# Kernel optimization log

Hardware: AMD Instinct MI355X
Metric: run time of the kernel (lower is better)

## Reference

```python
import jax, jax.numpy as jnp
import numpy as np

EPS = 1e-5

def setup_inputs() -> dict:
    key = jax.random.key(0)
    k1, k2, k3, k4, k5 = jax.random.split(key, 5)
    B, D, S = 4096, 2048, 16384
    return {
        "x": jax.random.normal(k1, (B, D), dtype=jnp.float32),
        "W_enc": jax.random.normal(k2, (S, D), dtype=jnp.float32) * 0.02,  # encoder.weight [n_sae, n_input]
        "W_dec": jax.random.normal(k3, (D, S), dtype=jnp.float32) * 0.02,  # decoder.weight [n_input, n_sae]
        "pre_bias": jax.random.normal(k4, (D,), dtype=jnp.float32) * 0.01,
        "sae_bias": jax.random.normal(k5, (S,), dtype=jnp.float32) * 0.01,
        "k": 64,
    }

def reference(x, W_enc, W_dec, pre_bias, sae_bias, k):
    # --- pre_process: layer norm (torch.std is unbiased -> ddof=1) ---
    x_mean = jnp.mean(x, axis=-1, keepdims=True)
    std = jnp.std(x, axis=-1, ddof=1, keepdims=True)
    x_ln = (x - x_mean) / (std + EPS)
    # --- encode: latents_pre = (x_ln - pre_bias) @ W_enc^T + sae_bias ---
    pre_activations = (x_ln - pre_bias) @ W_enc.T + sae_bias  # [B, n_sae]
    # --- TopK activation: keep top-k, ReLU them, zero the rest ---
    vals, idx = jax.lax.top_k(pre_activations, k)              # [B, k]
    vals = jax.nn.relu(vals)
    rows = jnp.arange(pre_activations.shape[0])[:, None]       # [B, 1]
    latents = jnp.zeros_like(pre_activations).at[rows, idx].set(vals)
    # --- decode + un-normalize ---
    recons = latents @ W_dec.T + pre_bias                      # [B, n_input]
    recons = recons * std + x_mean
    return pre_activations, latents, recons
```

## Files before the change

### kernel.cpp

```cpp
#include <hip/hip_runtime.h>
#include <cstdint>
#include <cstddef>

#define EPSV 1e-5f
#define CAP 224
#define PAD 16
#define DELTA 0.03f
#define AMBCAP 64

__device__ __forceinline__ unsigned short f2bf(float f) {
  unsigned u = __float_as_uint(f);
  unsigned r = (u + 0x7FFFu + ((u >> 16) & 1u)) >> 16;
  return (unsigned short)r;
}
__device__ __forceinline__ float bf2f(unsigned short h) {
  return __uint_as_float(((unsigned)h) << 16);
}

__global__ __launch_bounds__(256) void ln_kernel(const float* __restrict__ x,
    const float* __restrict__ pre_bias, float* __restrict__ a,
    unsigned short* __restrict__ A2,
    float* __restrict__ stats, int D) {
  const int b = blockIdx.x;
  const int tid = threadIdx.x;
  const float4* x4 = reinterpret_cast<const float4*>(x + (size_t)b * D);
  const float4* pb4 = reinterpret_cast<const float4*>(pre_bias);
  float4* a4 = reinterpret_cast<float4*>(a + (size_t)b * D);
  float4 v0 = x4[tid], v1 = x4[tid + 256];
  float s = v0.x + v0.y + v0.z + v0.w + v1.x + v1.y + v1.z + v1.w;
  float ss = v0.x*v0.x + v0.y*v0.y + v0.z*v0.z + v0.w*v0.w
           + v1.x*v1.x + v1.y*v1.y + v1.z*v1.z + v1.w*v1.w;
#pragma unroll
  for (int off = 1; off < 64; off <<= 1) { s += __shfl_xor(s, off); ss += __shfl_xor(ss, off); }
  __shared__ float wsum[4], wssq[4], bmean, bstd;
  int wave = tid >> 6;
  if ((tid & 63) == 0) { wsum[wave] = s; wssq[wave] = ss; }
  __syncthreads();
  if (tid == 0) {
    float S1 = wsum[0] + wsum[1] + wsum[2] + wsum[3];
    float S2 = wssq[0] + wssq[1] + wssq[2] + wssq[3];
    float mean = S1 / (float)D;
    float var = (S2 - (float)D * mean * mean) / (float)(D - 1);
    float sd = sqrtf(fmaxf(var, 0.f));
    bmean = mean; bstd = sd;
    stats[2*b] = mean; stats[2*b+1] = sd;
  }
  __syncthreads();
  float mean = bmean, rstd = 1.f / (bstd + EPSV);
  float4 p0 = pb4[tid], p1 = pb4[tid + 256];
  float4 o0, o1;
  o0.x = (v0.x - mean) * rstd - p0.x; o0.y = (v0.y - mean) * rstd - p0.y;
  o0.z = (v0.z - mean) * rstd - p0.z; o0.w = (v0.w - mean) * rstd - p0.w;
  o1.x = (v1.x - mean) * rstd - p1.x; o1.y = (v1.y - mean) * rstd - p1.y;
  o1.z = (v1.z - mean) * rstd - p1.z; o1.w = (v1.w - mean) * rstd - p1.w;
  a4[tid] = o0; a4[tid + 256] = o1;
  if (A2) {
    unsigned short* row = A2 + (size_t)b * 2048;
    ushort4 h0 = make_ushort4(f2bf(o0.x), f2bf(o0.y), f2bf(o0.z), f2bf(o0.w));
    ushort4 h1 = make_ushort4(f2bf(o1.x), f2bf(o1.y), f2bf(o1.z), f2bf(o1.w));
    *reinterpret_cast<ushort4*>(row + tid * 4) = h0;
    *reinterpret_cast<ushort4*>(row + 1024 + tid * 4) = h1;
  }
}

__global__ __launch_bounds__(256) void cvt_w_kernel(const float* __restrict__ W,
    unsigned short* __restrict__ W2, int D) {
  const int s = blockIdx.x, tid = threadIdx.x;
  const float4* w4 = reinterpret_cast<const float4*>(W + (size_t)s * D);
  unsigned short* row = W2 + (size_t)s * D;
  float4 v0 = w4[tid * 2], v1 = w4[tid * 2 + 1];
  uint4 p;
  p.x = (unsigned)f2bf(v0.x) | ((unsigned)f2bf(v0.y) << 16);
  p.y = (unsigned)f2bf(v0.z) | ((unsigned)f2bf(v0.w) << 16);
  p.z = (unsigned)f2bf(v1.x) | ((unsigned)f2bf(v1.y) << 16);
  p.w = (unsigned)f2bf(v1.z) | ((unsigned)f2bf(v1.w) << 16);
  *reinterpret_cast<uint4*>(row + tid * 8) = p;
}

typedef __attribute__((ext_vector_type(8))) short bf8;
typedef __attribute__((ext_vector_type(4))) float f32x4;

__device__ __forceinline__ void gload16(const void* g, void* l) {
  __builtin_amdgcn_global_load_lds(
      (const __attribute__((address_space(1))) unsigned int*)g,
      (__attribute__((address_space(3))) unsigned int*)l,
      16, 0, 0);
}

__global__ __launch_bounds__(512) void enc_gemm_bf16(
    const unsigned short* __restrict__ A2,
    const unsigned short* __restrict__ W2,
    const float* __restrict__ sae_bias,
    float* __restrict__ C, int M, int N) {
  __shared__ __align__(16) short As0[128 * 64];
  __shared__ __align__(16) short Bs0[128 * 64];
  __shared__ __align__(16) short As1[128 * 64];
  __shared__ __align__(16) short Bs1[128 * 64];
  const int tid = threadIdx.x;
  const int bn = blockIdx.x, bm = blockIdx.y;
  const int w = tid >> 6, l = tid & 63;

  const unsigned short* gA[2];
  const unsigned short* gB[2];
  int ldsSlot[2];
#pragma unroll
  for (int r = 0; r < 2; ++r) {
    int slot = r * 512 + tid;
    int row = slot >> 3, unit = slot & 7;
    int gcol = (unit ^ (row & 7)) * 8;
    gA[r] = A2 + (size_t)(bm * 128 + row) * 2048 + gcol;
    gB[r] = W2 + (size_t)(bn * 128 + row) * 2048 + gcol;
    ldsSlot[r] = slot * 8;
  }

  const int wm = (w >> 2) * 64, wn = (w & 3) * 32;
  const int r15 = l & 15, b7 = l & 7, u = l >> 4;
  const int colks0 = ((u + 0) ^ b7) * 8;
  const int colks1 = ((u + 4) ^ b7) * 8;
  const int baseA = (wm + r15) * 64;
  const int baseB = (wn + r15) * 64;

  f32x4 acc[4][2];
#pragma unroll
  for (int mi = 0; mi < 4; ++mi)
#pragma unroll
    for (int ni = 0; ni < 2; ++ni) acc[mi][ni] = (f32x4){0.f, 0.f, 0.f, 0.f};

#define STAGE(Adst, Bdst, koff)                                   \
  {                                                               \
    _Pragma("unroll")                                             \
    for (int r = 0; r < 2; ++r) {                                 \
      gload16(gA[r] + (koff), &(Adst)[ldsSlot[r]]);               \
      gload16(gB[r] + (koff), &(Bdst)[ldsSlot[r]]);               \
    }                                                             \
  }

#define COMPUTE(Asrc, Bsrc)                                       \
  {                                                               \
    _Pragma("unroll")                                             \
    for (int ks = 0; ks < 2; ++ks) {                              \
      const int ck = ks ? colks1 : colks0;                        \
      bf8 af[4], bfv[2];                                          \
      _Pragma("unroll")                                           \
      for (int mi = 0; mi < 4; ++mi)                              \
        af[mi] = *reinterpret_cast<const bf8*>(&(Asrc)[baseA + mi * 1024 + ck]); \
      _Pragma("unroll")                                           \
      for (int ni = 0; ni < 2; ++ni)                              \
        bfv[ni] = *reinterpret_cast<const bf8*>(&(Bsrc)[baseB + ni * 1024 + ck]); \
      __builtin_amdgcn_s_setprio(1);                              \
      _Pragma("unroll")                                           \
      for (int mi = 0; mi < 4; ++mi)                              \
        _Pragma("unroll")                                         \
        for (int ni = 0; ni < 2; ++ni)                            \
          acc[mi][ni] = __builtin_amdgcn_mfma_f32_16x16x32_bf16(  \
              af[mi], bfv[ni], acc[mi][ni], 0, 0, 0);             \
      __builtin_amdgcn_s_setprio(0);                              \
    }                                                             \
  }

#define SYNC_TILE()                                               \
  {                                                               \
    asm volatile("s_waitcnt vmcnt(0)" ::: "memory");              \
    __builtin_amdgcn_s_barrier();                                 \
    asm volatile("" ::: "memory");                                \
  }

  STAGE(As0, Bs0, 0);
  SYNC_TILE();

  for (int t = 0; t < 32; t += 2) {
    STAGE(As1, Bs1, (t + 1) * 64);
    COMPUTE(As0, Bs0);
    SYNC_TILE();
    if (t + 2 < 32) STAGE(As0, Bs0, (t + 2) * 64);
    COMPUTE(As1, Bs1);
    SYNC_TILE();
  }
#undef STAGE
#undef COMPUTE
#undef SYNC_TILE

  const int cm = (l >> 4) * 4, cn = l & 15;
  float sb[2];
#pragma unroll
  for (int ni = 0; ni < 2; ++ni)
    sb[ni] = sae_bias[bn * 128 + wn + ni * 16 + cn];
#pragma unroll
  for (int mi = 0; mi < 4; ++mi) {
#pragma unroll
    for (int r = 0; r < 4; ++r) {
      int row = bm * 128 + wm + mi * 16 + cm + r;
      float* Crow = C + (size_t)row * N + bn * 128 + wn;
#pragma unroll
      for (int ni = 0; ni < 2; ++ni)
        Crow[ni * 16 + cn] = acc[mi][ni][r] + sb[ni];
    }
  }
}

#define BM 128
#define BN 128
#define BK 32
#define LDP 136

__global__ __launch_bounds__(256) void enc_gemm_f32(
    const float* __restrict__ A, const float* __restrict__ Bw,
    const float* __restrict__ sae_bias, float* __restrict__ C,
    int M, int N, int K) {
  __shared__ __align__(16) float As[BK * LDP];
  __shared__ __align__(16) float Bs[BK * LDP];
  const int tid = threadIdx.x;
  const int bn = blockIdx.x, bm = blockIdx.y;
  const float* Ab = A + (size_t)bm * BM * K;
  const float* Bb = Bw + (size_t)bn * BN * K;
  float acc[8][8];
#pragma unroll
  for (int i = 0; i < 8; ++i)
#pragma unroll
    for (int j = 0; j < 8; ++j) acc[i][j] = 0.f;
  const int tn = tid & 15, tm = tid >> 4;
  const int lk = tid & 31;
  const int lm4 = (tid >> 5) * 4;
  for (int k0 = 0; k0 < K; k0 += BK) {
#pragma unroll
    for (int i = 0; i < 4; ++i) {
      int mb = i * 32 + lm4;
      float a0 = Ab[(size_t)(mb + 0) * K + k0 + lk];
      float a1 = Ab[(size_t)(mb + 1) * K + k0 + lk];
      float a2 = Ab[(size_t)(mb + 2) * K + k0 + lk];
      float a3 = Ab[(size_t)(mb + 3) * K + k0 + lk];
      *reinterpret_cast<float4*>(&As[lk * LDP + mb]) = make_float4(a0, a1, a2, a3);
      float b0 = Bb[(size_t)(mb + 0) * K + k0 + lk];
      float b1 = Bb[(size_t)(mb + 1) * K + k0 + lk];
      float b2 = Bb[(size_t)(mb + 2) * K + k0 + lk];
      float b3 = Bb[(size_t)(mb + 3) * K + k0 + lk];
      *reinterpret_cast<float4*>(&Bs[lk * LDP + mb]) = make_float4(b0, b1, b2, b3);
    }
    __syncthreads();
#pragma unroll 8
    for (int kk = 0; kk < BK; ++kk) {
      float4 a0 = *reinterpret_cast<const float4*>(&As[kk * LDP + tm * 4]);
      float4 a1 = *reinterpret_cast<const float4*>(&As[kk * LDP + tm * 4 + 64]);
      float4 b0 = *reinterpret_cast<const float4*>(&Bs[kk * LDP + tn * 4]);
      float4 b1 = *reinterpret_cast<const float4*>(&Bs[kk * LDP + tn * 4 + 64]);
      float av[8] = {a0.x, a0.y, a0.z, a0.w, a1.x, a1.y, a1.z, a1.w};
      float bv[8] = {b0.x, b0.y, b0.z, b0.w, b1.x, b1.y, b1.z, b1.w};
#pragma unroll
      for (int ii = 0; ii < 8; ++ii)
#pragma unroll
        for (int jj = 0; jj < 8; ++jj)
          acc[ii][jj] = fmaf(av[ii], bv[jj], acc[ii][jj]);
    }
    __syncthreads();
  }
  float4 sb0 = *reinterpret_cast<const float4*>(sae_bias + bn * BN + tn * 4);
  float4 sb1 = *reinterpret_cast<const float4*>(sae_bias + bn * BN + tn * 4 + 64);
#pragma unroll
  for (int ii = 0; ii < 8; ++ii) {
    int row = bm * BM + (ii < 4 ? tm * 4 + ii : 64 + tm * 4 + ii - 4);
    float* Crow = C + (size_t)row * N + bn * BN;
    float4 o0 = make_float4(acc[ii][0] + sb0.x, acc[ii][1] + sb0.y,
                            acc[ii][2] + sb0.z, acc[ii][3] + sb0.w);
    float4 o1 = make_float4(acc[ii][4] + sb1.x, acc[ii][5] + sb1.y,
                            acc[ii][6] + sb1.z, acc[ii][7] + sb1.w);
    *reinterpret_cast<float4*>(Crow + tn * 4) = o0;
    *reinterpret_cast<float4*>(Crow + tn * 4 + 64) = o1;
  }
}

__device__ __forceinline__ unsigned mapf(float f) {
  unsigned u = __float_as_uint(f);
  return (u & 0x80000000u) ? ~u : (u | 0x80000000u);
}

__global__ __launch_bounds__(256) void topk_select(
    const float* __restrict__ preact, float* __restrict__ latents,
    const int* __restrict__ kp, int* __restrict__ cand, float* __restrict__ candv,
    int* __restrict__ candcnt, int S) {
  const int b = blockIdx.x, tid = threadIdx.x;
  const float4* row4 = reinterpret_cast<const float4*>(preact + (size_t)b * S);
  __shared__ int hist[4096];
  __shared__ int tsum[256];
  __shared__ unsigned sh_pref, sh_thr;
  __shared__ int sh_done, sh_cum, sh_cnt;
  int K = kp[0]; if (K > 192) K = 192;
  const int r = K + PAD;
  if (tid == 0) { sh_done = 0; sh_pref = 0; sh_cum = 0; }
  for (int level = 0; level < 3; ++level) {
    __syncthreads();
    if (sh_done) break;
    const int shift = (level == 0) ? 20 : (level == 1) ? 8 : 0;
    const int width = (level == 2) ? 8 : 12;
    const int nb = 1 << width;
    const unsigned mask = (unsigned)nb - 1;
    for (int i = tid; i < nb; i += 256) hist[i] = 0;
    __syncthreads();
    const unsigned pref = sh_pref;
    for (int i = tid; i < S / 4; i += 256) {
      float4 v = row4[i];
      unsigned uu[4] = {mapf(v.x), mapf(v.y), mapf(v.z), mapf(v.w)};
#pragma unroll
      for (int q = 0; q < 4; ++q) {
        bool ok = (level == 0) || ((uu[q] >> (shift + width)) == pref);
        if (ok) atomicAdd(&hist[(uu[q] >> shift) & mask], 1);
      }
    }
    __syncthreads();
    const int per = nb >> 8;
    int myts = 0;
#pragma unroll 4
    for (int j = 0; j < per; ++j) myts += hist[tid * per + j];
    tsum[tid] = myts;
    __syncthreads();
    for (int o = 1; o < 256; o <<= 1) {
      int v_ = (tid + o < 256) ? tsum[tid + o] : 0;
      __syncthreads();
      tsum[tid] += v_;
      __syncthreads();
    }
    const int rr = r - sh_cum;
    const int sufIncl = tsum[tid];
    const int sufExcl = sufIncl - myts;
    if (sufExcl < rr && rr <= sufIncl) {
      int running = sufExcl;
      for (int j = per - 1; j >= 0; --j) {
        int bb = tid * per + j;
        int c = hist[bb];
        if (running + c >= rr) {
          unsigned npref = (sh_pref << width) | (unsigned)bb;
          int candTotal = sh_cum + running + c;
          sh_pref = npref;
          sh_cum += running;
          if (candTotal <= CAP || level == 2) { sh_thr = npref << shift; sh_done = 1; }
          break;
        }
        running += c;
      }
    }
  }
  __syncthreads();
  const unsigned T = sh_thr;
  if (tid == 0) sh_cnt = 0;
  __syncthreads();
  float4* lat4 = reinterpret_cast<float4*>(latents + (size_t)b * S);
  float4 z = make_float4(0.f, 0.f, 0.f, 0.f);
  for (int i = tid; i < S / 4; i += 256) {
    float4 v = row4[i];
    unsigned uu[4] = {mapf(v.x), mapf(v.y), mapf(v.z), mapf(v.w)};
    float vv[4] = {v.x, v.y, v.z, v.w};
#pragma unroll
    for (int q = 0; q < 4; ++q) {
      if (uu[q] >= T) {
        int p = atomicAdd(&sh_cnt, 1);
        if (p < CAP) { cand[(size_t)b * CAP + p] = i * 4 + q; candv[(size_t)b * CAP + p] = vv[q]; }
      }
    }
    lat4[i] = z;
  }
  __syncthreads();
  if (tid == 0) candcnt[b] = (sh_cnt < CAP) ? sh_cnt : CAP;
}

__global__ __launch_bounds__(256) void topk_refine(
    const float* __restrict__ a, const float* __restrict__ W_enc,
    const float* __restrict__ sae_bias, const int* __restrict__ kp,
    const int* __restrict__ cand, const float* __restrict__ candv,
    const int* __restrict__ candcnt,
    float* __restrict__ latents, int* __restrict__ out_idx, float* __restrict__ out_val,
    int D, int S) {
  const int b = blockIdx.x, tid = threadIdx.x;
  __shared__ float sv[256];
  __shared__ int si[256];
  __shared__ double sv64[256];
  __shared__ double av[AMBCAP];
  __shared__ int agid[AMBCAP];
  __shared__ int sh_amb, sh_nin;
  int K = kp[0]; if (K > 192) K = 192;
  const int cnt = candcnt[b];
  const int wave = tid >> 6, lane = tid & 63;
  const float4* ar4 = reinterpret_cast<const float4*>(a + (size_t)b * D);
  const int nit = D / 256;

  if (tid < cnt) { sv[tid] = candv[(size_t)b * CAP + tid]; si[tid] = cand[(size_t)b * CAP + tid]; }
  else { sv[tid] = -3.0e38f; si[tid] = 0x7FFFFFFF; }
  __syncthreads();
  for (int ksz = 2; ksz <= 256; ksz <<= 1) {
    for (int j = ksz >> 1; j > 0; j >>= 1) {
      int ixj = tid ^ j;
      if (ixj > tid) {
        float v1 = sv[tid], v2 = sv[ixj];
        int i1 = si[tid], i2 = si[ixj];
        bool dirDesc = ((tid & ksz) == 0);
        bool firstBetter = (v1 > v2) || (v1 == v2 && i1 < i2);
        if (dirDesc ? (!firstBetter) : firstBetter) {
          sv[tid] = v2; sv[ixj] = v1; si[tid] = i2; si[ixj] = i1;
        }
      }
      __syncthreads();
    }
  }
  const float vK = sv[K - 1];
  if (tid == 0) { sh_amb = 0; sh_nin = 0; }
  __syncthreads();
  bool isC = tid < cnt;
  if (isC && (sv[tid] > vK + DELTA)) atomicAdd(&sh_nin, 1);
  if (isC && fabsf(sv[tid] - vK) <= DELTA) {
    int p = atomicAdd(&sh_amb, 1);
    if (p < AMBCAP) agid[p] = si[tid];
  }
  __syncthreads();
  const int nAmb = sh_amb, nIn = sh_nin;

  if (nAmb <= AMBCAP) {
    for (int c = wave; c < nAmb; c += 4) {
      int sidx = agid[c];
      const float4* wr4 = reinterpret_cast<const float4*>(W_enc + (size_t)sidx * D);
      double acc = 0.0;
      for (int m = 0; m < nit; ++m) {
        float4 a_ = ar4[m * 64 + lane];
        float4 w_ = wr4[m * 64 + lane];
        acc += (double)a_.x * w_.x + (double)a_.y * w_.y
             + (double)a_.z * w_.z + (double)a_.w * w_.w;
      }
#pragma unroll
      for (int off = 1; off < 64; off <<= 1) acc += __shfl_xor(acc, off);
      if (lane == 0) av[c] = acc + (double)sae_bias[sidx];
    }
    __syncthreads();
    if (tid < AMBCAP && tid >= nAmb) { av[tid] = -1.0e300; agid[tid] = 0x7FFFFFFF; }
    __syncthreads();
    for (int ksz = 2; ksz <= AMBCAP; ksz <<= 1) {
      for (int j = ksz >> 1; j > 0; j >>= 1) {
        int ixj = tid ^ j;
        if (tid < AMBCAP && ixj > tid) {
          double v1 = av[tid], v2 = av[ixj];
          int i1 = agid[tid], i2 = agid[ixj];
          bool dirDesc = ((tid & ksz) == 0);
          bool firstBetter = (v1 > v2) || (v1 == v2 && i1 < i2);
          if (dirDesc ? (!firstBetter) : firstBetter) {
            av[tid] = v2; av[ixj] = v1; agid[tid] = i2; agid[ixj] = i1;
          }
        }
        __syncthreads();
      }
    }
    if (tid < K) {
      int gidx; float val;
      if (tid < nIn) { gidx = si[tid]; val = sv[tid]; }
      else { int c = tid - nIn; gidx = agid[c]; val = (float)av[c]; }
      val = fmaxf(val, 0.f);
      latents[(size_t)b * S + gidx] = val;
      out_idx[(size_t)b * 256 + tid] = gidx;
      out_val[(size_t)b * 256 + tid] = val;
    }
  } else {
    for (int c = wave; c < cnt; c += 4) {
      int sidx = si[c];
      const float4* wr4 = reinterpret_cast<const float4*>(W_enc + (size_t)sidx * D);
      double acc = 0.0;
      for (int m = 0; m < nit; ++m) {
        float4 a_ = ar4[m * 64 + lane];
        float4 w_ = wr4[m * 64 + lane];
        acc += (double)a_.x * w_.x + (double)a_.y * w_.y
             + (double)a_.z * w_.z + (double)a_.w * w_.w;
      }
#pragma unroll
      for (int off = 1; off < 64; off <<= 1) acc += __shfl_xor(acc, off);
      if (lane == 0) sv64[c] = acc + (double)sae_bias[sidx];
    }
    __syncthreads();
    if (tid >= cnt) { sv64[tid] = -1.0e300; si[tid] = 0x7FFFFFFF; }
    __syncthreads();
    for (int ksz = 2; ksz <= 256; ksz <<= 1) {
      for (int j = ksz >> 1; j > 0; j >>= 1) {
        int ixj = tid ^ j;
        if (ixj > tid) {
          double v1 = sv64[tid], v2 = sv64[ixj];
          int i1 = si[tid], i2 = si[ixj];
          bool dirDesc = ((tid & ksz) == 0);
          bool firstBetter = (v1 > v2) || (v1 == v2 && i1 < i2);
          if (dirDesc ? (!firstBetter) : firstBetter) {
            sv64[tid] = v2; sv64[ixj] = v1; si[tid] = i2; si[ixj] = i1;
          }
        }
        __syncthreads();
      }
    }
    if (tid < K) {
      int idx = si[tid];
      float rv = fmaxf((float)sv64[tid], 0.f);
      latents[(size_t)b * S + idx] = rv;
      out_idx[(size_t)b * 256 + tid] = idx;
      out_val[(size_t)b * 256 + tid] = rv;
    }
  }
}

__global__ __launch_bounds__(256) void transpose_cvt(const float* __restrict__ src,
    unsigned short* __restrict__ dst, int D, int S) {
  __shared__ float t[32][33];
  int s0 = blockIdx.x * 32, d0 = blockIdx.y * 32;
  int tx = threadIdx.x & 31, ty = threadIdx.x >> 5;
#pragma unroll
  for (int i = 0; i < 32; i += 8)
    t[ty + i][tx] = src[(size_t)(d0 + ty + i) * S + s0 + tx];
  __syncthreads();
#pragma unroll
  for (int i = 0; i < 32; i += 8)
    dst[(size_t)(s0 + ty + i) * D + d0 + tx] = f2bf(t[tx][ty + i]);
}

__global__ __launch_bounds__(512) void decode_bf16(
    const unsigned short* __restrict__ WdTh, const float* __restrict__ pre_bias,
    const float* __restrict__ stats, const int* __restrict__ kp,
    const int* __restrict__ out_idx, const float* __restrict__ out_val,
    float* __restrict__ recons, int D) {
  const int b = blockIdx.x, tid = threadIdx.x;
  __shared__ int sidx[192];
  __shared__ float sval[192];
  int K = kp[0]; if (K > 192) K = 192;
  if (tid < K) { sidx[tid] = out_idx[(size_t)b * 256 + tid]; sval[tid] = out_val[(size_t)b * 256 + tid]; }
  __syncthreads();
  const int c0 = tid * 4;
  float4 p0 = *reinterpret_cast<const float4*>(pre_bias + c0);
  float acc0 = p0.x, acc1 = p0.y, acc2 = p0.z, acc3 = p0.w;
  for (int j = 0; j < K; ++j) {
    float v = sval[j];
    uint2 wv = *reinterpret_cast<const uint2*>(WdTh + (size_t)sidx[j] * D + c0);
    acc0 = fmaf(v, bf2f((unsigned short)(wv.x & 0xffff)), acc0);
    acc1 = fmaf(v, bf2f((unsigned short)(wv.x >> 16)),    acc1);
    acc2 = fmaf(v, bf2f((unsigned short)(wv.y & 0xffff)), acc2);
    acc3 = fmaf(v, bf2f((unsigned short)(wv.y >> 16)),    acc3);
  }
  float mean = stats[2 * b], sd = stats[2 * b + 1];
  float4 o = make_float4(acc0 * sd + mean, acc1 * sd + mean,
                         acc2 * sd + mean, acc3 * sd + mean);
  *reinterpret_cast<float4*>(recons + (size_t)b * D + c0) = o;
}

__global__ __launch_bounds__(256) void decode_fb(
    const float* __restrict__ Wd, const float* __restrict__ pre_bias,
    const float* __restrict__ stats, const int* __restrict__ kp,
    const int* __restrict__ out_idx, const float* __restrict__ out_val,
    float* __restrict__ recons, int D, int S) {
  const int b = blockIdx.x, tid = threadIdx.x;
  __shared__ int sidx[192];
  __shared__ float sval[192];
  int K = kp[0]; if (K > 192) K = 192;
  if (tid < K) { sidx[tid] = out_idx[(size_t)b * 256 + tid]; sval[tid] = out_val[(size_t)b * 256 + tid]; }
  __syncthreads();
  for (int d = tid; d < D; d += 256) {
    float acc = pre_bias[d];
    for (int j = 0; j < K; ++j)
      acc = fmaf(sval[j], Wd[(size_t)d * S + sidx[j]], acc);
    recons[(size_t)b * D + d] = acc * stats[2 * b + 1] + stats[2 * b];
  }
}

extern "C" void kernel_launch(void* const* d_in, const int* in_sizes, int n_in,
                              void* d_out, int out_size, void* d_ws, size_t ws_size,
                              hipStream_t stream) {
  const float* x        = (const float*)d_in[0];
  const float* W_enc    = (const float*)d_in[1];
  const float* W_dec    = (const float*)d_in[2];
  const float* pre_bias = (const float*)d_in[3];
  const float* sae_bias = (const float*)d_in[4];
  const int*   kp       = (const int*)d_in[5];
  const int D = in_sizes[3];
  const int S = in_sizes[4];
  const int B = in_sizes[0] / D;

  float* out_pre = (float*)d_out;
  float* out_lat = out_pre + (size_t)B * S;
  float* out_rec = out_lat + (size_t)B * S;

  char* ws = (char*)d_ws;
  size_t off = 0;
  float* a = (float*)(ws + off);        off += (size_t)B * D * 4;
  float* stats = (float*)(ws + off);    off += (size_t)B * 2 * 4;
  int* cand = (int*)(ws + off);         off += (size_t)B * CAP * 4;
  float* candv = (float*)(ws + off);    off += (size_t)B * CAP * 4;
  int* candcnt = (int*)(ws + off);      off += (size_t)B * 4;
  int* oidx = (int*)(ws + off);         off += (size_t)B * 256 * 4;
  float* oval = (float*)(ws + off);     off += (size_t)B * 256 * 4;
  off = (off + 255) & ~(size_t)255;
  unsigned short* A2 = (unsigned short*)(ws + off);
  size_t offW2 = off + (size_t)B * D * 2;
  unsigned short* W2 = (unsigned short*)(ws + offW2);
  size_t offWdT = offW2 + (size_t)S * D * 2;
  unsigned short* WdTh = (unsigned short*)(ws + offWdT);
  size_t offEnd = offWdT + (size_t)S * D * 2;
  bool useBf16 = (D == 2048) && (B % 128 == 0) && (S % 128 == 0) &&
                 (S % 32 == 0) && (D % 32 == 0) && (ws_size >= offEnd);

  if (useBf16) {
    ln_kernel<<<B, 256, 0, stream>>>(x, pre_bias, a, A2, stats, D);
    cvt_w_kernel<<<S, 256, 0, stream>>>(W_enc, W2, D);
    enc_gemm_bf16<<<dim3(S / 128, B / 128), 512, 0, stream>>>(A2, W2, sae_bias, out_pre, B, S);
    transpose_cvt<<<dim3(S / 32, D / 32), 256, 0, stream>>>(W_dec, WdTh, D, S);
    topk_select<<<B, 256, 0, stream>>>(out_pre, out_lat, kp, cand, candv, candcnt, S);
    topk_refine<<<B, 256, 0, stream>>>(a, W_enc, sae_bias, kp, cand, candv, candcnt,
                                       out_lat, oidx, oval, D, S);
    decode_bf16<<<B, 512, 0, stream>>>(WdTh, pre_bias, stats, kp, oidx, oval, out_rec, D);
  } else {
    ln_kernel<<<B, 256, 0, stream>>>(x, pre_bias, a, nullptr, stats, D);
    enc_gemm_f32<<<dim3(S / BN, B / BM), 256, 0, stream>>>(a, W_enc, sae_bias, out_pre, B, S, D);
    topk_select<<<B, 256, 0, stream>>>(out_pre, out_lat, kp, cand, candv, candcnt, S);
    topk_refine<<<B, 256, 0, stream>>>(a, W_enc, sae_bias, kp, cand, candv, candcnt,
                                       out_lat, oidx, oval, D, S);
    decode_fb<<<B, 256, 0, stream>>>(W_dec, pre_bias, stats, kp, oidx, oval, out_rec, D, S);
  }
}
```

Measured before the change: 850.7 us.

## Load encoder GEMM A operand directly from global into registers, bypassing LDS

The encoder GEMM no longer stages the activation (A) tile through shared memory. Each wave now reads its A fragments straight from global memory into registers inside the compute step, while the weight (B) tile is still double-buffered in LDS. This halves LDS use per block, and the launch bounds now request 4 blocks per CU to raise occupancy. The cost is that the four waves sharing the same rows each load A redundantly, the 64-byte-per-row access pattern coalesces poorly, and the global-load latency now sits inside the compute loop behind a full vmcnt(0) wait.

```diff
diff --git a/kernel.cpp b/kernel.cpp
--- a/kernel.cpp
+++ b/kernel.cpp
@@ -87,20 +87,17 @@
       16, 0, 0);
 }
 
-__global__ __launch_bounds__(512) void enc_gemm_bf16(
+__global__ __launch_bounds__(512, 4) void enc_gemm_bf16(
     const unsigned short* __restrict__ A2,
     const unsigned short* __restrict__ W2,
     const float* __restrict__ sae_bias,
     float* __restrict__ C, int M, int N) {
-  __shared__ __align__(16) short As0[128 * 64];
   __shared__ __align__(16) short Bs0[128 * 64];
-  __shared__ __align__(16) short As1[128 * 64];
   __shared__ __align__(16) short Bs1[128 * 64];
   const int tid = threadIdx.x;
   const int bn = blockIdx.x, bm = blockIdx.y;
   const int w = tid >> 6, l = tid & 63;
 
-  const unsigned short* gA[2];
   const unsigned short* gB[2];
   int ldsSlot[2];
 #pragma unroll
@@ -108,7 +105,6 @@
     int slot = r * 512 + tid;
     int row = slot >> 3, unit = slot & 7;
     int gcol = (unit ^ (row & 7)) * 8;
-    gA[r] = A2 + (size_t)(bm * 128 + row) * 2048 + gcol;
     gB[r] = W2 + (size_t)(bn * 128 + row) * 2048 + gcol;
     ldsSlot[r] = slot * 8;
   }
@@ -117,43 +113,58 @@
   const int r15 = l & 15, b7 = l & 7, u = l >> 4;
   const int colks0 = ((u + 0) ^ b7) * 8;
   const int colks1 = ((u + 4) ^ b7) * 8;
-  const int baseA = (wm + r15) * 64;
   const int baseB = (wn + r15) * 64;
 
+  const unsigned short* gA = A2 + (size_t)(bm * 128 + wm + r15) * 2048 + u * 8;
+
   f32x4 acc[4][2];
 #pragma unroll
   for (int mi = 0; mi < 4; ++mi)
 #pragma unroll
     for (int ni = 0; ni < 2; ++ni) acc[mi][ni] = (f32x4){0.f, 0.f, 0.f, 0.f};
 
-#define STAGE(Adst, Bdst, koff)                                   \
+#define STAGEB(Bdst, koff)                                        \
   {                                                               \
     _Pragma("unroll")                                             \
-    for (int r = 0; r < 2; ++r) {                                 \
-      gload16(gA[r] + (koff), &(Adst)[ldsSlot[r]]);               \
+    for (int r = 0; r < 2; ++r)                                   \
       gload16(gB[r] + (koff), &(Bdst)[ldsSlot[r]]);               \
-    }                                                             \
-  }
-
-#define COMPUTE(Asrc, Bsrc)                                       \
+  }
+
+#define COMPUTE(Bsrc, koff)                                       \
   {                                                               \
+    bf8 af0[4], af1[4];                                           \
     _Pragma("unroll")                                             \
-    for (int ks = 0; ks < 2; ++ks) {                              \
-      const int ck = ks ? colks1 : colks0;                        \
-      bf8 af[4], bfv[2];                                          \
-      _Pragma("unroll")                                           \
-      for (int mi = 0; mi < 4; ++mi)                              \
-        af[mi] = *reinterpret_cast<const bf8*>(&(Asrc)[baseA + mi * 1024 + ck]); \
+    for (int mi = 0; mi < 4; ++mi)                                \
+      af0[mi] = *reinterpret_cast<const bf8*>(gA + (size_t)(mi * 16) * 2048 + (koff)); \
+    _Pragma("unroll")                                             \
+    for (int mi = 0; mi < 4; ++mi)                                \
+      af1[mi] = *reinterpret_cast<const bf8*>(gA + (size_t)(mi * 16) * 2048 + (koff) + 32); \
+    {                                                             \
+      bf8 bfv[2];                                                 \
       _Pragma("unroll")                                           \
       for (int ni = 0; ni < 2; ++ni)                              \
-        bfv[ni] = *reinterpret_cast<const bf8*>(&(Bsrc)[baseB + ni * 1024 + ck]); \
+        bfv[ni] = *reinterpret_cast<const bf8*>(&(Bsrc)[baseB + ni * 1024 + colks0]); \
       __builtin_amdgcn_s_setprio(1);                              \
       _Pragma("unroll")                                           \
       for (int mi = 0; mi < 4; ++mi)                              \
         _Pragma("unroll")                                         \
         for (int ni = 0; ni < 2; ++ni)                            \
           acc[mi][ni] = __builtin_amdgcn_mfma_f32_16x16x32_bf16(  \
-              af[mi], bfv[ni], acc[mi][ni], 0, 0, 0);             \
+              af0[mi], bfv[ni], acc[mi][ni], 0, 0, 0);            \
+      __builtin_amdgcn_s_setprio(0);                              \
+    }                                                             \
+    {                                                             \
+      bf8 bfv[2];                                                 \
+      _Pragma("unroll")                                           \
+      for (int ni = 0; ni < 2; ++ni)                              \
+        bfv[ni] = *reinterpret_cast<const bf8*>(&(Bsrc)[baseB + ni * 1024 + colks1]); \
+      __builtin_amdgcn_s_setprio(1);                              \
+      _Pragma("unroll")                                           \
+      for (int mi = 0; mi < 4; ++mi)                              \
+        _Pragma("unroll")                                         \
+        for (int ni = 0; ni < 2; ++ni)                            \
+          acc[mi][ni] = __builtin_amdgcn_mfma_f32_16x16x32_bf16(  \
+              af1[mi], bfv[ni], acc[mi][ni], 0, 0, 0);            \
       __builtin_amdgcn_s_setprio(0);                              \
     }                                                             \
   }
@@ -165,18 +176,18 @@
     asm volatile("" ::: "memory");                                \
   }
 
-  STAGE(As0, Bs0, 0);
+  STAGEB(Bs0, 0);
   SYNC_TILE();
 
   for (int t = 0; t < 32; t += 2) {
-    STAGE(As1, Bs1, (t + 1) * 64);
-    COMPUTE(As0, Bs0);
+    STAGEB(Bs1, (t + 1) * 64);
+    COMPUTE(Bs0, t * 64);
     SYNC_TILE();
-    if (t + 2 < 32) STAGE(As0, Bs0, (t + 2) * 64);
-    COMPUTE(As1, Bs1);
+    if (t + 2 < 32) STAGEB(Bs0, (t + 2) * 64);
+    COMPUTE(Bs1, (t + 1) * 64);
     SYNC_TILE();
   }
-#undef STAGE
+#undef STAGEB
 #undef COMPUTE
 #undef SYNC_TILE
 
```

Result: slower. 1.554 ms (+82.7%).
